# Kernel optimization log

Measured on AMD Instinct MI355X. Metric: run time of the kernel, lower is better.

## Reference

```python
import jax, jax.numpy as jnp
import numpy as np

B, S, H = 1, 4096, 2048
NH, HD = 16, 128
ROPE_N = 32
WINDOW = 1024
EPS = 1e-5


def _build_rope(seq_len, n_elem, base=10000.0):
    theta = 1.0 / (base ** (np.arange(0, n_elem, 2, dtype=np.float32) / n_elem))  # [n_elem/2]
    idx = np.arange(seq_len, dtype=np.float32)
    freqs = np.outer(idx, theta)                     # [S, n_elem/2]
    freqs = np.concatenate([freqs, freqs], axis=-1)  # [S, n_elem]
    return jnp.asarray(np.cos(freqs)), jnp.asarray(np.sin(freqs))


def setup_inputs() -> dict:
    key = jax.random.key(0)
    k1, k2, k3 = jax.random.split(key, 3)
    x = jax.random.normal(k1, (B, S, H), dtype=jnp.float32)
    cos, sin = _build_rope(S, ROPE_N)
    norm_weight = jnp.ones((H,), dtype=jnp.float32)
    qkv_w = jax.random.normal(k2, (3 * H, H), dtype=jnp.float32) * (1.0 / np.sqrt(H))
    o_w = jax.random.normal(k3, (H, H), dtype=jnp.float32) * (1.0 / np.sqrt(H))
    return {"x": x, "cos": cos, "sin": sin, "norm_weight": norm_weight,
            "qkv_w": qkv_w, "o_w": o_w}


def _apply_rope(t, cos, sin):
    # t: [B, NH, S, ROPE_N]; cos/sin: [S, ROPE_N]
    half = t.shape[-1] // 2
    x1, x2 = t[..., :half], t[..., half:]
    rotated = jnp.concatenate([-x2, x1], axis=-1)
    return t * cos + rotated * sin


def reference(x, cos, sin, norm_weight, qkv_w, o_w):
    b, s, h = x.shape
    # RMSNorm (computed in fp32)
    xf = x.astype(jnp.float32)
    ms = jnp.mean(xf * xf, axis=-1, keepdims=True)
    xn = (norm_weight * (xf * jax.lax.rsqrt(ms + EPS))).astype(x.dtype)
    # fused QKV projection
    qkv = jnp.einsum('bsh,oh->bso', xn, qkv_w)  # [B, S, 3H]
    q, k, v = jnp.split(qkv, 3, axis=-1)
    def to_heads(t):
        return t.reshape(b, s, NH, HD).transpose(0, 2, 1, 3)  # [B, NH, S, HD]
    q, k, v = to_heads(q), to_heads(k), to_heads(v)
    # partial RoPE on first ROPE_N dims
    q = jnp.concatenate([_apply_rope(q[..., :ROPE_N], cos, sin), q[..., ROPE_N:]], axis=-1)
    k = jnp.concatenate([_apply_rope(k[..., :ROPE_N], cos, sin), k[..., ROPE_N:]], axis=-1)
    # sliding-window causal attention: query i attends keys j with i-WINDOW <= j <= i
    scale = 1.0 / np.sqrt(HD)
    scores = jnp.einsum('bnqd,bnkd->bnqk', q, k) * scale  # [B, NH, S, S]
    i = jnp.arange(s)[:, None]
    j = jnp.arange(s)[None, :]
    mask = (j <= i) & (j >= i - WINDOW)
    scores = jnp.where(mask, scores, jnp.finfo(scores.dtype).min)
    attn = jax.nn.softmax(scores, axis=-1)
    out = jnp.einsum('bnqk,bnkd->bnqd', attn, v)  # [B, NH, S, HD]
    out = out.transpose(0, 2, 1, 3).reshape(b, s, h)
    return jnp.einsum('bsh,oh->bso', out, o_w)
```

## Files before the change

kernel.cpp:

```cpp
#include <hip/hip_runtime.h>
#include <stdint.h>

#define S_LEN 4096
#define HDIM  2048
#define NHEAD 16
#define HD    128
#define WIN   1024

typedef float  f32x4  __attribute__((ext_vector_type(4)));
typedef float  f32x4v __attribute__((ext_vector_type(4)));
typedef __bf16 bf16x8 __attribute__((ext_vector_type(8)));
typedef short  short8 __attribute__((ext_vector_type(8)));
typedef short  short4v __attribute__((ext_vector_type(4)));

static __device__ __forceinline__ short f2bf(float f) {
  union { float f; uint32_t u; } v; v.f = f;
  uint32_t r = (v.u + 0x7FFFu + ((v.u >> 16) & 1u)) >> 16;
  return (short)(uint16_t)r;
}

static __device__ __forceinline__ void gload_lds16(const void* g, void* l) {
  __builtin_amdgcn_global_load_lds((__attribute__((address_space(1))) void*)g,
                                   (__attribute__((address_space(3))) void*)l,
                                   16, 0, 0);
}

__global__ __launch_bounds__(256) void rmsnorm_k(const float* __restrict__ x,
                                                 const float* __restrict__ w,
                                                 short* __restrict__ xn) {
  const int row = blockIdx.x;
  const int t = threadIdx.x;
  const float* xr = x + (size_t)row * HDIM;
  f32x4v a = *(const f32x4v*)&xr[t * 8];
  f32x4v b = *(const f32x4v*)&xr[t * 8 + 4];
  float ss = a.x*a.x + a.y*a.y + a.z*a.z + a.w*a.w
           + b.x*b.x + b.y*b.y + b.z*b.z + b.w*b.w;
#pragma unroll
  for (int d = 1; d < 64; d <<= 1) ss += __shfl_xor(ss, d, 64);
  __shared__ float sred[4];
  if ((t & 63) == 0) sred[t >> 6] = ss;
  __syncthreads();
  float tot = sred[0] + sred[1] + sred[2] + sred[3];
  float rs = rsqrtf(tot * (1.0f / HDIM) + 1e-5f);
  float vv[8] = {a.x, a.y, a.z, a.w, b.x, b.y, b.z, b.w};
  const float* wp = w + t * 8;
  short8 o;
#pragma unroll
  for (int j = 0; j < 8; ++j) o[j] = f2bf(vv[j] * rs * wp[j]);
  *(short8*)&xn[(size_t)row * HDIM + t * 8] = o;
}

__global__ __launch_bounds__(256) void cvt_k(const float* __restrict__ in,
                                             short* __restrict__ out, int n4) {
  int i = blockIdx.x * 256 + threadIdx.x;
  if (i >= n4) return;
  f32x4v v = *(const f32x4v*)&in[(size_t)i * 4];
  short4v o = { f2bf(v.x), f2bf(v.y), f2bf(v.z), f2bf(v.w) };
  *(short4v*)&out[(size_t)i * 4] = o;
}

template <int EPI>
__global__ __launch_bounds__(512) void gemm_p(
    const short* __restrict__ A, const short* __restrict__ Bt,
    int M, int N, int K, float* __restrict__ Cf,
    const float* __restrict__ cosb, const float* __restrict__ sinb,
    short* __restrict__ Qo, short* __restrict__ Ko, short* __restrict__ Vt) {
  __shared__ __align__(16) short lds[3][24576];
  const int t = threadIdx.x;
  const int wid = t >> 6, l = t & 63;
  const int lr = l & 15, lg = l >> 4;
  const int wm = wid >> 1, wn = wid & 1;

  int bid = blockIdx.x;
  const int nwg = gridDim.x;
  bid = (bid & 7) * (nwg >> 3) + (bid >> 3);
  const int nbx = N >> 7;
  const int bx = bid % nbx, by = bid / nbx;
  const int brow = by * 256, bcol = bx * 128;

  const int srow7 = (t >> 3) & 7;
  const int scol = ((t & 7) ^ srow7) * 8;

  f32x4 acc[4][4] = {};

  const int nt = K >> 6;

#define STAGE_A(slot, kt, i)                                                     \
  gload_lds16(A + (size_t)(brow + (i) * 64 + (t >> 3)) * K + (kt) + scol,        \
              &lds[slot][(i) * 4096 + t * 8])
#define STAGE_B(slot, kt, i)                                                     \
  gload_lds16(Bt + (size_t)(bcol + (i) * 64 + (t >> 3)) * K + (kt) + scol,       \
              &lds[slot][16384 + (i) * 4096 + t * 8])

  STAGE_A(0, 0, 0); STAGE_A(0, 0, 1); STAGE_A(0, 0, 2); STAGE_A(0, 0, 3);
  STAGE_B(0, 0, 0); STAGE_B(0, 0, 1);
  STAGE_A(1, 64, 0); STAGE_A(1, 64, 1); STAGE_A(1, 64, 2); STAGE_A(1, 64, 3);
  STAGE_B(1, 64, 0); STAGE_B(1, 64, 1);
  asm volatile("s_waitcnt vmcnt(6)" ::: "memory");
  __builtin_amdgcn_s_barrier();

  const int xo0 = ((lg ^ (lr & 7)) << 3);
  const int xo1 = (((4 + lg) ^ (lr & 7)) << 3);

  int slot = 0;
  for (int tt = 0; tt < nt; ++tt) {
    const int s2 = (slot + 2 >= 3) ? slot - 1 : slot + 2;
    const int kt2 = (tt + 2) << 6;
    const bool st = (tt + 2 < nt);
    bf16x8 af[4], bfr[4];

#pragma unroll
    for (int m = 0; m < 4; ++m)
      af[m] = *(const bf16x8*)&lds[slot][(wm * 64 + m * 16 + lr) * 64 + xo0];
#pragma unroll
    for (int n = 0; n < 4; ++n)
      bfr[n] = *(const bf16x8*)&lds[slot][16384 + (wn * 64 + n * 16 + lr) * 64 + xo0];
    if (st) { STAGE_A(s2, kt2, 0); STAGE_A(s2, kt2, 1); STAGE_B(s2, kt2, 0); }
    __builtin_amdgcn_s_barrier();
    asm volatile("s_waitcnt lgkmcnt(0)" ::: "memory");
    __builtin_amdgcn_sched_barrier(0);
    __builtin_amdgcn_s_setprio(1);
#pragma unroll
    for (int m = 0; m < 4; ++m)
#pragma unroll
      for (int n = 0; n < 4; ++n)
        acc[m][n] = __builtin_amdgcn_mfma_f32_16x16x32_bf16(af[m], bfr[n], acc[m][n], 0, 0, 0);
    __builtin_amdgcn_s_setprio(0);
    __builtin_amdgcn_s_barrier();

#pragma unroll
    for (int m = 0; m < 4; ++m)
      af[m] = *(const bf16x8*)&lds[slot][(wm * 64 + m * 16 + lr) * 64 + xo1];
#pragma unroll
    for (int n = 0; n < 4; ++n)
      bfr[n] = *(const bf16x8*)&lds[slot][16384 + (wn * 64 + n * 16 + lr) * 64 + xo1];
    if (st) { STAGE_A(s2, kt2, 2); STAGE_A(s2, kt2, 3); STAGE_B(s2, kt2, 1); }
    if (tt < nt - 2) asm volatile("s_waitcnt vmcnt(6)" ::: "memory");
    else             asm volatile("s_waitcnt vmcnt(0)" ::: "memory");
    __builtin_amdgcn_s_barrier();
    asm volatile("s_waitcnt lgkmcnt(0)" ::: "memory");
    __builtin_amdgcn_sched_barrier(0);
    __builtin_amdgcn_s_setprio(1);
#pragma unroll
    for (int m = 0; m < 4; ++m)
#pragma unroll
      for (int n = 0; n < 4; ++n)
        acc[m][n] = __builtin_amdgcn_mfma_f32_16x16x32_bf16(af[m], bfr[n], acc[m][n], 0, 0, 0);
    __builtin_amdgcn_s_setprio(0);
    __builtin_amdgcn_s_barrier();

    slot = (slot + 1 >= 3) ? 0 : slot + 1;
  }
#undef STAGE_A
#undef STAGE_B

  const int row0 = brow + wm * 64, col0 = bcol + wn * 64;
  if (EPI == 0) {
#pragma unroll
    for (int m = 0; m < 4; ++m)
#pragma unroll
      for (int n = 0; n < 4; ++n)
#pragma unroll
        for (int r = 0; r < 4; ++r)
          Cf[(size_t)(row0 + m * 16 + lg * 4 + r) * N + col0 + n * 16 + lr] = acc[m][n][r];
  } else {
    const int sec = col0 >> 11;
    const int headc = (col0 & 2047) >> 7;
    const bool rope = (sec < 2) && ((col0 & 127) == 0);
#pragma unroll
    for (int m = 0; m < 4; ++m) {
#pragma unroll
      for (int r = 0; r < 4; ++r) {
        const int s = row0 + m * 16 + lg * 4 + r;
        float v0 = acc[m][0][r], v1 = acc[m][1][r];
        float v2 = acc[m][2][r], v3 = acc[m][3][r];
        if (rope) {
          const int d0 = lr;
          float c0 = cosb[s * 32 + d0],      sn0 = sinb[s * 32 + d0];
          float c1 = cosb[s * 32 + d0 + 16], sn1 = sinb[s * 32 + d0 + 16];
          float t0 = v0 * c0 - v1 * sn0;
          float t1 = v1 * c1 + v0 * sn1;
          v0 = t0; v1 = t1;
        }
        float vv[4] = {v0, v1, v2, v3};
#pragma unroll
        for (int n = 0; n < 4; ++n) {
          const int col = col0 + n * 16 + lr;
          const int d = col & 127;
          if (sec == 0)
            Qo[((size_t)headc * S_LEN + s) * HD + d] = f2bf(vv[n] * 0.08838834764831845f);
          else if (sec == 1)
            Ko[((size_t)headc * S_LEN + s) * HD + d] = f2bf(vv[n]);
          else
            Vt[((size_t)headc * HD + d) * S_LEN + s] = f2bf(vv[n]);
        }
      }
    }
  }
}

__global__ __launch_bounds__(256) void attn_k(const short* __restrict__ Q,
                                              const short* __restrict__ Kk,
                                              const short* __restrict__ Vt,
                                              short* __restrict__ Ao) {
  __shared__ __align__(16) short Kl[2][64 * HD];
  __shared__ __align__(16) short Vl[2][HD * 64];
  __shared__ __align__(16) short Pl[4][16 * 72];
  const int head = blockIdx.y;
  int bxx = blockIdx.x;
  bxx = ((bxx & 7) << 3) | (bxx >> 3);
  const int qb = bxx * 64;
  const int w = threadIdx.x >> 6, l = threadIdx.x & 63;
  const int lr = l & 15, lg = l >> 4;
  const int q0w = qb + w * 16;
  const short* Qh = Q  + (size_t)head * S_LEN * HD;
  const short* Kh = Kk + (size_t)head * S_LEN * HD;
  const short* Vh = Vt + (size_t)head * HD * S_LEN;

  bf16x8 qf[4];
#pragma unroll
  for (int kk = 0; kk < 4; ++kk)
    qf[kk] = *(const bf16x8*)&Qh[(size_t)(q0w + lr) * HD + kk * 32 + lg * 8];

  f32x4 oacc[8] = {};
  float mrow[4], lrow[4];
#pragma unroll
  for (int r = 0; r < 4; ++r) { mrow[r] = -1e30f; lrow[r] = 0.0f; }

  const int k_begin = (qb >= WIN) ? (qb - WIN) : 0;
  const int nt = (qb + 64 - k_begin) >> 6;
  const int swz = (lr & 7) << 4;

#define STAGE_KV(p, k0) do {                                                   \
    _Pragma("unroll")                                                          \
    for (int i = 0; i < 4; ++i) {                                              \
      const int row = i * 16 + w * 4 + (l >> 4);                               \
      gload_lds16(Kh + (size_t)((k0) + row) * HD + (((l & 15) ^ (row & 7)) * 8),\
                  &Kl[p][(i * 16 + w * 4) * HD]);                              \
    }                                                                          \
    _Pragma("unroll")                                                          \
    for (int i = 0; i < 4; ++i) {                                              \
      const int row = i * 32 + w * 8 + (l >> 3);                               \
      gload_lds16(Vh + (size_t)row * S_LEN + (k0) + (((l & 7) ^ (row & 7)) * 8),\
                  &Vl[p][(i * 32 + w * 8) * 64]);                              \
    }                                                                          \
  } while (0)

  STAGE_KV(0, k_begin);
  asm volatile("s_waitcnt vmcnt(0)" ::: "memory");
  __syncthreads();

  for (int tkv = 0; tkv < nt; ++tkv) {
    const int k0 = k_begin + tkv * 64;
    const int pl = tkv & 1;
    if (tkv + 1 < nt) STAGE_KV(pl ^ 1, k0 + 64);

    f32x4 sacc[4] = {};
#pragma unroll
    for (int nf = 0; nf < 4; ++nf) {
      const char* kb = (const char*)&Kl[pl][0] + (nf * 16 + lr) * 256;
      bf16x8 kf[4];
#pragma unroll
      for (int kk = 0; kk < 4; ++kk)
        kf[kk] = *(const bf16x8*)(kb + ((kk * 64 + lg * 16) ^ swz));
#pragma unroll
      for (int kk = 0; kk < 4; ++kk)
        sacc[nf] = __builtin_amdgcn_mfma_f32_16x16x32_bf16(qf[kk], kf[kk], sacc[nf], 0, 0, 0);
    }

    const bool full = (k0 + 63 <= q0w) && (k0 >= q0w + 15 - WIN);
    float scl[4];
#pragma unroll
    for (int r = 0; r < 4; ++r) {
      const int i = q0w + lg * 4 + r;
      float sv[4];
#pragma unroll
      for (int nf = 0; nf < 4; ++nf) sv[nf] = sacc[nf][r];
      if (!full) {
#pragma unroll
        for (int nf = 0; nf < 4; ++nf) {
          const int j = k0 + nf * 16 + lr;
          if (!((j <= i) && (j + WIN >= i))) sv[nf] = -1e30f;
        }
      }
      float mx = fmaxf(fmaxf(sv[0], sv[1]), fmaxf(sv[2], sv[3]));
#pragma unroll
      for (int d = 1; d < 16; d <<= 1) mx = fmaxf(mx, __shfl_xor(mx, d, 64));
      const float mn = fmaxf(mrow[r], mx);
      const float sc = __expf(mrow[r] - mn);
      mrow[r] = mn;
      float p[4], rs = 0.0f;
#pragma unroll
      for (int nf = 0; nf < 4; ++nf) { p[nf] = __expf(sv[nf] - mn); rs += p[nf]; }
#pragma unroll
      for (int d = 1; d < 16; d <<= 1) rs += __shfl_xor(rs, d, 64);
      lrow[r] = lrow[r] * sc + rs;
      scl[r] = sc;
#pragma unroll
      for (int nf = 0; nf < 4; ++nf)
        Pl[w][(lg * 4 + r) * 72 + nf * 16 + lr] = f2bf(p[nf]);
    }
#pragma unroll
    for (int df = 0; df < 8; ++df)
#pragma unroll
      for (int r = 0; r < 4; ++r) oacc[df][r] *= scl[r];

    bf16x8 pa[2];
#pragma unroll
    for (int kk2 = 0; kk2 < 2; ++kk2)
      pa[kk2] = *(const bf16x8*)&Pl[w][lr * 72 + kk2 * 32 + lg * 8];

#pragma unroll
    for (int df = 0; df < 8; ++df) {
      const char* vb = (const char*)&Vl[pl][0] + (df * 16 + lr) * 128;
#pragma unroll
      for (int kk2 = 0; kk2 < 2; ++kk2) {
        bf16x8 vfrag = *(const bf16x8*)(vb + ((kk2 * 64 + lg * 16) ^ swz));
        oacc[df] = __builtin_amdgcn_mfma_f32_16x16x32_bf16(pa[kk2], vfrag, oacc[df], 0, 0, 0);
      }
    }

    if (tkv + 1 < nt) asm volatile("s_waitcnt vmcnt(0)" ::: "memory");
    __syncthreads();
  }
#undef STAGE_KV

  float inv[4];
#pragma unroll
  for (int r = 0; r < 4; ++r) inv[r] = 1.0f / lrow[r];
#pragma unroll
  for (int df = 0; df < 8; ++df)
#pragma unroll
    for (int r = 0; r < 4; ++r) {
      const int s = q0w + lg * 4 + r;
      Ao[(size_t)s * HDIM + head * HD + df * 16 + lr] = f2bf(oacc[df][r] * inv[r]);
    }
}

extern "C" void kernel_launch(void* const* d_in, const int* in_sizes, int n_in,
                              void* d_out, int out_size, void* d_ws, size_t ws_size,
                              hipStream_t stream) {
  const float* x    = (const float*)d_in[0];
  const float* cosb = (const float*)d_in[1];
  const float* sinb = (const float*)d_in[2];
  const float* nw   = (const float*)d_in[3];
  const float* qkvw = (const float*)d_in[4];
  const float* ow   = (const float*)d_in[5];
  float* out = (float*)d_out;

  short* ws = (short*)d_ws;
  short* xn = ws;
  short* wb = xn + (size_t)S_LEN * HDIM;
  short* Qb = wb + (size_t)3 * HDIM * HDIM;
  short* Kb = Qb + (size_t)NHEAD * S_LEN * HD;
  short* Vb = Kb + (size_t)NHEAD * S_LEN * HD;
  short* Ao = xn;

  rmsnorm_k<<<S_LEN, 256, 0, stream>>>(x, nw, xn);
  cvt_k<<<(3 * HDIM * HDIM / 4 + 255) / 256, 256, 0, stream>>>(qkvw, wb, 3 * HDIM * HDIM / 4);
  gemm_p<1><<<(3 * HDIM / 128) * (S_LEN / 256), 512, 0, stream>>>(
      xn, wb, S_LEN, 3 * HDIM, HDIM, nullptr, cosb, sinb, Qb, Kb, Vb);
  cvt_k<<<(HDIM * HDIM / 4 + 255) / 256, 256, 0, stream>>>(ow, wb, HDIM * HDIM / 4);
  attn_k<<<dim3(S_LEN / 64, NHEAD), 256, 0, stream>>>(Qb, Kb, Vb, Ao);
  gemm_p<0><<<(HDIM / 128) * (S_LEN / 256), 512, 0, stream>>>(
      Ao, wb, S_LEN, HDIM, HDIM, out, nullptr, nullptr, nullptr, nullptr, nullptr);
}
```

Measured before the change: 310.8 us.

## Halve GEMM k-step to shrink LDS and raise occupancy; add MFMA priority hints in attention

The GEMM pipeline moves from a 64-wide k tile to a 32-wide one. This halves the triple-buffered LDS footprint, and launch bounds now request four waves per SIMD so more workgroups can be resident per CU. The per-iteration body is simplified to one LDS fragment load and one MFMA block, with a 4-way swizzle and precomputed source pointers. In the attention kernel, s_setprio is raised around the QK and PV MFMA groups to favour matrix issue. The trade-off is twice as many barriers and waitcnt points per unit of K, with less latency hiding per stage.

```diff
diff --git a/kernel.cpp b/kernel.cpp
--- a/kernel.cpp
+++ b/kernel.cpp
@@ -60,12 +60,12 @@
 }
 
 template <int EPI>
-__global__ __launch_bounds__(512) void gemm_p(
+__global__ __launch_bounds__(512, 4) void gemm_p(
     const short* __restrict__ A, const short* __restrict__ Bt,
     int M, int N, int K, float* __restrict__ Cf,
     const float* __restrict__ cosb, const float* __restrict__ sinb,
     short* __restrict__ Qo, short* __restrict__ Ko, short* __restrict__ Vt) {
-  __shared__ __align__(16) short lds[3][24576];
+  __shared__ __align__(16) short lds[3][12288];
   const int t = threadIdx.x;
   const int wid = t >> 6, l = t & 63;
   const int lr = l & 15, lg = l >> 4;
@@ -78,64 +78,42 @@
   const int bx = bid % nbx, by = bid / nbx;
   const int brow = by * 256, bcol = bx * 128;
 
-  const int srow7 = (t >> 3) & 7;
-  const int scol = ((t & 7) ^ srow7) * 8;
+  const int scol = ((t & 3) ^ ((t >> 2) & 3)) * 8;
+  const short* As = A  + (size_t)(brow + (t >> 2)) * K + scol;
+  const short* Bs = Bt + (size_t)(bcol + (t >> 2)) * K + scol;
 
   f32x4 acc[4][4] = {};
 
-  const int nt = K >> 6;
-
-#define STAGE_A(slot, kt, i)                                                     \
-  gload_lds16(A + (size_t)(brow + (i) * 64 + (t >> 3)) * K + (kt) + scol,        \
-              &lds[slot][(i) * 4096 + t * 8])
-#define STAGE_B(slot, kt, i)                                                     \
-  gload_lds16(Bt + (size_t)(bcol + (i) * 64 + (t >> 3)) * K + (kt) + scol,       \
-              &lds[slot][16384 + (i) * 4096 + t * 8])
-
-  STAGE_A(0, 0, 0); STAGE_A(0, 0, 1); STAGE_A(0, 0, 2); STAGE_A(0, 0, 3);
-  STAGE_B(0, 0, 0); STAGE_B(0, 0, 1);
-  STAGE_A(1, 64, 0); STAGE_A(1, 64, 1); STAGE_A(1, 64, 2); STAGE_A(1, 64, 3);
-  STAGE_B(1, 64, 0); STAGE_B(1, 64, 1);
-  asm volatile("s_waitcnt vmcnt(6)" ::: "memory");
+  const int ns = K >> 5;
+
+#define STAGE(slot, kt) do {                                                \
+    gload_lds16(As + (size_t)(kt),           &lds[slot][t * 8]);            \
+    gload_lds16(As + (size_t)128 * K + (kt), &lds[slot][4096 + t * 8]);     \
+    gload_lds16(Bs + (size_t)(kt),           &lds[slot][8192 + t * 8]);     \
+  } while (0)
+
+  STAGE(0, 0);
+  STAGE(1, 32);
+  asm volatile("s_waitcnt vmcnt(3)" ::: "memory");
   __builtin_amdgcn_s_barrier();
 
-  const int xo0 = ((lg ^ (lr & 7)) << 3);
-  const int xo1 = (((4 + lg) ^ (lr & 7)) << 3);
+  const int xo = ((lg ^ (lr & 3)) << 3);
+  const int arow = (wm * 64 + lr) * 32;
+  const int brow_s = 8192 + (wn * 64 + lr) * 32;
 
   int slot = 0;
-  for (int tt = 0; tt < nt; ++tt) {
+  for (int ss = 0; ss < ns; ++ss) {
     const int s2 = (slot + 2 >= 3) ? slot - 1 : slot + 2;
-    const int kt2 = (tt + 2) << 6;
-    const bool st = (tt + 2 < nt);
     bf16x8 af[4], bfr[4];
 
 #pragma unroll
     for (int m = 0; m < 4; ++m)
-      af[m] = *(const bf16x8*)&lds[slot][(wm * 64 + m * 16 + lr) * 64 + xo0];
+      af[m] = *(const bf16x8*)&lds[slot][arow + m * 512 + xo];
 #pragma unroll
     for (int n = 0; n < 4; ++n)
-      bfr[n] = *(const bf16x8*)&lds[slot][16384 + (wn * 64 + n * 16 + lr) * 64 + xo0];
-    if (st) { STAGE_A(s2, kt2, 0); STAGE_A(s2, kt2, 1); STAGE_B(s2, kt2, 0); }
-    __builtin_amdgcn_s_barrier();
-    asm volatile("s_waitcnt lgkmcnt(0)" ::: "memory");
-    __builtin_amdgcn_sched_barrier(0);
-    __builtin_amdgcn_s_setprio(1);
-#pragma unroll
-    for (int m = 0; m < 4; ++m)
-#pragma unroll
-      for (int n = 0; n < 4; ++n)
-        acc[m][n] = __builtin_amdgcn_mfma_f32_16x16x32_bf16(af[m], bfr[n], acc[m][n], 0, 0, 0);
-    __builtin_amdgcn_s_setprio(0);
-    __builtin_amdgcn_s_barrier();
-
-#pragma unroll
-    for (int m = 0; m < 4; ++m)
-      af[m] = *(const bf16x8*)&lds[slot][(wm * 64 + m * 16 + lr) * 64 + xo1];
-#pragma unroll
-    for (int n = 0; n < 4; ++n)
-      bfr[n] = *(const bf16x8*)&lds[slot][16384 + (wn * 64 + n * 16 + lr) * 64 + xo1];
-    if (st) { STAGE_A(s2, kt2, 2); STAGE_A(s2, kt2, 3); STAGE_B(s2, kt2, 1); }
-    if (tt < nt - 2) asm volatile("s_waitcnt vmcnt(6)" ::: "memory");
+      bfr[n] = *(const bf16x8*)&lds[slot][brow_s + n * 512 + xo];
+    if (ss + 2 < ns) STAGE(s2, (ss + 2) << 5);
+    if (ss < ns - 2) asm volatile("s_waitcnt vmcnt(3)" ::: "memory");
     else             asm volatile("s_waitcnt vmcnt(0)" ::: "memory");
     __builtin_amdgcn_s_barrier();
     asm volatile("s_waitcnt lgkmcnt(0)" ::: "memory");
@@ -151,8 +129,7 @@
 
     slot = (slot + 1 >= 3) ? 0 : slot + 1;
   }
-#undef STAGE_A
-#undef STAGE_B
+#undef STAGE
 
   const int row0 = brow + wm * 64, col0 = bcol + wn * 64;
   if (EPI == 0) {
@@ -263,9 +240,11 @@
 #pragma unroll
       for (int kk = 0; kk < 4; ++kk)
         kf[kk] = *(const bf16x8*)(kb + ((kk * 64 + lg * 16) ^ swz));
+      __builtin_amdgcn_s_setprio(1);
 #pragma unroll
       for (int kk = 0; kk < 4; ++kk)
         sacc[nf] = __builtin_amdgcn_mfma_f32_16x16x32_bf16(qf[kk], kf[kk], sacc[nf], 0, 0, 0);
+      __builtin_amdgcn_s_setprio(0);
     }
 
     const bool full = (k0 + 63 <= q0w) && (k0 >= q0w + 15 - WIN);
@@ -313,11 +292,12 @@
 #pragma unroll
     for (int df = 0; df < 8; ++df) {
       const char* vb = (const char*)&Vl[pl][0] + (df * 16 + lr) * 128;
-#pragma unroll
-      for (int kk2 = 0; kk2 < 2; ++kk2) {
-        bf16x8 vfrag = *(const bf16x8*)(vb + ((kk2 * 64 + lg * 16) ^ swz));
-        oacc[df] = __builtin_amdgcn_mfma_f32_16x16x32_bf16(pa[kk2], vfrag, oacc[df], 0, 0, 0);
-      }
+      bf16x8 vfrag0 = *(const bf16x8*)(vb + ((0 * 64 + lg * 16) ^ swz));
+      bf16x8 vfrag1 = *(const bf16x8*)(vb + ((1 * 64 + lg * 16) ^ swz));
+      __builtin_amdgcn_s_setprio(1);
+      oacc[df] = __builtin_amdgcn_mfma_f32_16x16x32_bf16(pa[0], vfrag0, oacc[df], 0, 0, 0);
+      oacc[df] = __builtin_amdgcn_mfma_f32_16x16x32_bf16(pa[1], vfrag1, oacc[df], 0, 0, 0);
+      __builtin_amdgcn_s_setprio(0);
     }
 
     if (tkv + 1 < nt) asm volatile("s_waitcnt vmcnt(0)" ::: "memory");
```

After: 323.5 us. 1.04x slower.
